# Kernel tuning notes

Hardware: AMD Instinct MI355X
Metric: run time of the kernel (lower is better)

The kernel has to match this reference:

```python
import jax, jax.numpy as jnp
import numpy as np

EMBED = 1024
HEADS = 16
HEAD_DIM = EMBED // HEADS


def setup_inputs() -> dict:
    key = jax.random.key(0)
    k1, k2, k3, k4, k5, k6 = jax.random.split(key, 6)
    N, S = 4, 2048
    return {
        "values": jax.random.normal(k1, (N, S, EMBED), dtype=jnp.float32),
        "keys": jax.random.normal(k2, (N, S, EMBED), dtype=jnp.float32),
        "query": jax.random.normal(k3, (N, S, EMBED), dtype=jnp.float32),
        "mask": jax.random.randint(k4, (N, 1, S, S), 0, 2, dtype=jnp.int32),
        "W_out": jax.random.normal(k5, (EMBED, EMBED), dtype=jnp.float32) * (1.0 / np.sqrt(EMBED)),
        "b_out": jax.random.normal(k6, (EMBED,), dtype=jnp.float32) * 0.01,
    }


def reference(values, keys, query, mask, W_out, b_out):
    N, Q = query.shape[0], query.shape[1]
    K = keys.shape[1]
    v = values.reshape(N, K, HEADS, HEAD_DIM)
    k = keys.reshape(N, K, HEADS, HEAD_DIM)
    q = query.reshape(N, Q, HEADS, HEAD_DIM)
    # [N,H,Q,K] score matrix (materialized, as in the original)
    energy = jnp.einsum("nqhd,nkhd->nhqk", q, k)
    energy = jnp.where(mask == 0, jnp.float32(-1e20), energy)
    # NOTE: original scales by sqrt(embed_size), not sqrt(head_dim)
    attn = jax.nn.softmax(energy / jnp.sqrt(jnp.float32(EMBED)), axis=3)
    out = jnp.einsum("nhqk,nkhd->nqhd", attn, v).reshape(N, Q, EMBED)
    return out @ W_out.T + b_out
```

## Files before the change

### kernel.cpp

```cpp
#include <hip/hip_runtime.h>
#include <stdint.h>

#define SEQ 2048
#define NB 4
#define NHD 16
#define HD 64
#define EMB 1024

typedef unsigned short u16;
typedef unsigned int u32;
typedef unsigned long long u64;
typedef __bf16 bf16x8 __attribute__((ext_vector_type(8)));
typedef float f32x4 __attribute__((ext_vector_type(4)));

__device__ __forceinline__ u16 f2bf(float f) {
    u32 u = __builtin_bit_cast(u32, f);
    u32 r = u + 0x7FFFu + ((u >> 16) & 1u);
    return (u16)(r >> 16);
}

__device__ __forceinline__ float exp2_hw(float x) {
    float r;
    asm("v_exp_f32 %0, %1" : "=v"(r) : "v"(x));
    return r;
}

__device__ __forceinline__ u32 cvtpk_bf16(float lo, float hi) {
    u32 r;
    asm("v_cvt_pk_bf16_f32 %0, %1, %2" : "=v"(r) : "v"(lo), "v"(hi));
    return r;
}

__device__ __forceinline__ void gld16(const void* g, void* l) {
    __builtin_amdgcn_global_load_lds(
        (const __attribute__((address_space(1))) u32*)g,
        (__attribute__((address_space(3))) u32*)l, 16, 0, 0);
}

__global__ void prep_qk(const float* __restrict__ q, const float* __restrict__ k,
                        u16* __restrict__ qb, u16* __restrict__ kb) {
    int tid = blockIdx.x * 256 + threadIdx.x;
    int unit = tid >> 4;
    int dq = (tid & 15) << 2;
    int h = unit & (NHD - 1);
    int ns = unit >> 4;
    int n = ns >> 11, s = ns & (SEQ - 1);
    size_t src = (size_t)ns * EMB + h * HD + dq;
    float4 qv = *(const float4*)(q + src);
    float4 kv = *(const float4*)(k + src);
    size_t dst = ((size_t)(n * NHD + h) * SEQ + s) * HD + dq;
    const float QS = 0.04508422f;
    ushort4 qo, ko;
    qo.x = f2bf(qv.x * QS); qo.y = f2bf(qv.y * QS);
    qo.z = f2bf(qv.z * QS); qo.w = f2bf(qv.w * QS);
    ko.x = f2bf(kv.x); ko.y = f2bf(kv.y); ko.z = f2bf(kv.z); ko.w = f2bf(kv.w);
    *(ushort4*)(qb + dst) = qo;
    *(ushort4*)(kb + dst) = ko;
}

__global__ void prep_v(const float* __restrict__ v, u16* __restrict__ vt) {
    __shared__ float t[64][65];
    int s0 = blockIdx.x << 6, h = blockIdx.y, n = blockIdx.z;
    int tid = threadIdx.x;
    int c = (tid & 15) << 2;
    int r0 = tid >> 4;
#pragma unroll
    for (int it = 0; it < 4; it++) {
        int r = r0 + (it << 4);
        float4 val = *(const float4*)(v + ((size_t)n * SEQ + s0 + r) * EMB + h * HD + c);
        t[c][r] = val.x; t[c + 1][r] = val.y; t[c + 2][r] = val.z; t[c + 3][r] = val.w;
    }
    __syncthreads();
    int d = tid >> 2, so = (tid & 3) << 4;
    size_t dst = ((size_t)(n * NHD + h) * HD + d) * SEQ + s0 + so;
#pragma unroll
    for (int j = 0; j < 4; j++) {
        ushort4 o;
        o.x = f2bf(t[d][so + 4 * j + 0]); o.y = f2bf(t[d][so + 4 * j + 1]);
        o.z = f2bf(t[d][so + 4 * j + 2]); o.w = f2bf(t[d][so + 4 * j + 3]);
        *(ushort4*)(vt + dst + 4 * j) = o;
    }
}

__global__ void prep_mask(const int* __restrict__ m, u64* __restrict__ mb) {
    int gw = (blockIdx.x * 256 + threadIdx.x) >> 6;
    int lane = threadIdx.x & 63;
    int src = ((lane & 12) << 2) | ((lane & 48) >> 2) | (lane & 3);
    for (int i = 0; i < 64; i++) {
        size_t widx = (size_t)gw * 64 + i;
        int v = m[widx * 64 + src];
        u64 b = __ballot(v != 0);
        if (lane == 0) mb[widx] = b;
    }
}

__global__ void prep_w(const float* __restrict__ w, u16* __restrict__ wb) {
    int tid = blockIdx.x * 256 + threadIdx.x;
    float4 v = *(const float4*)(w + (size_t)tid * 4);
    ushort4 o;
    o.x = f2bf(v.x); o.y = f2bf(v.y); o.z = f2bf(v.z); o.w = f2bf(v.w);
    *(ushort4*)(wb + (size_t)tid * 4) = o;
}

__global__ __launch_bounds__(256, 4) void attn_k(
    const u16* __restrict__ qb, const u16* __restrict__ kb,
    const u16* __restrict__ vt, const u64* __restrict__ mbits,
    u16* __restrict__ ao)
{
    __shared__ __align__(16) u16 lds_k[2][64 * 64];
    __shared__ __align__(16) u16 lds_v[2][64 * 64];
    __shared__ __align__(16) u16 lds_p[4][16 * 64];
    const int tid = threadIdx.x;
    const int wave = tid >> 6, lane = tid & 63;
    const int g = lane >> 4, c16 = lane & 15;
    const int bid = blockIdx.x;
    const int swz = (bid & 7) * 256 + (bid >> 3);
    const int n = swz >> 9, h = (swz >> 5) & 15, qt = swz & 31;
    const int qw = (qt << 6) + (wave << 4);
    const size_t nh = (size_t)(n * NHD + h);
    const u16* Qp = qb + nh * SEQ * HD;
    const u16* Kp = kb + nh * SEQ * HD;
    const u16* Vp = vt + nh * HD * SEQ;
    const u64* mrow = mbits + ((size_t)n * SEQ + qw + c16) * (SEQ / 64);

    bf16x8 qa0 = *(const bf16x8*)(Qp + (size_t)(qw + c16) * HD + 8 * g);
    bf16x8 qa1 = *(const bf16x8*)(Qp + (size_t)(qw + c16) * HD + 8 * g + 32);

    f32x4 o[4];
#pragma unroll
    for (int i = 0; i < 4; i++) o[i] = (f32x4){0.f, 0.f, 0.f, 0.f};
    float m_r = -INFINITY, l_r = 0.f;

    auto STAGE = [&](int buf, int kt) {
        int k0 = kt << 6;
#pragma unroll
        for (int i = 0; i < 2; i++) {
            int off = (i << 8) + tid;
            int row = off >> 3;
            int sch = (off & 7) ^ (row & 7);
            int ldso = ((i << 8) + (wave << 6)) << 3;
            gld16(Kp + (size_t)(k0 + row) * HD + (sch << 3), &lds_k[buf][ldso]);
            gld16(Vp + (size_t)row * SEQ + k0 + (sch << 3), &lds_v[buf][ldso]);
        }
    };

    auto COMPUTE = [&](int buf, int kt) {
        u64 mw_cur = mrow[kt];
        u32 mloc = (u32)(mw_cur >> (g << 4)) & 0xFFFFu;
        f32x4 s[4];
#pragma unroll
        for (int t = 0; t < 4; t++)
#pragma unroll
            for (int r = 0; r < 4; r++)
                s[t][r] = ((mloc >> ((t << 2) | r)) & 1u) ? 0.f : -1e20f;
#pragma unroll
        for (int t = 0; t < 4; t++) {
            int kc = (t << 4) + c16;
            int sw = (kc & 7) << 3;
            bf16x8 kf0 = *(const bf16x8*)&lds_k[buf][kc * 64 + ((8 * g) ^ sw)];
            bf16x8 kf1 = *(const bf16x8*)&lds_k[buf][kc * 64 + ((8 * g + 32) ^ sw)];
            s[t] = __builtin_amdgcn_mfma_f32_16x16x32_bf16(kf0, qa0, s[t], 0, 0, 0);
            s[t] = __builtin_amdgcn_mfma_f32_16x16x32_bf16(kf1, qa1, s[t], 0, 0, 0);
        }
        float pmax = fmaxf(fmaxf(fmaxf(s[0][0], s[0][1]), fmaxf(s[0][2], s[0][3])),
                           fmaxf(fmaxf(s[1][0], s[1][1]), fmaxf(s[1][2], s[1][3])));
        pmax = fmaxf(pmax, fmaxf(fmaxf(fmaxf(s[2][0], s[2][1]), fmaxf(s[2][2], s[2][3])),
                                 fmaxf(fmaxf(s[3][0], s[3][1]), fmaxf(s[3][2], s[3][3]))));
        pmax = fmaxf(pmax, __shfl_xor(pmax, 16));
        pmax = fmaxf(pmax, __shfl_xor(pmax, 32));
        if (__ballot(pmax > m_r + 8.f)) {
            float mnew = fmaxf(m_r, pmax);
            float sc = exp2_hw(m_r - mnew);
            m_r = mnew;
            l_r *= sc;
#pragma unroll
            for (int dt = 0; dt < 4; dt++) o[dt] *= sc;
        }
        float ladd = 0.f;
        u32 pk[4][2];
#pragma unroll
        for (int t = 0; t < 4; t++) {
            float p0 = exp2_hw(s[t][0] - m_r);
            float p1 = exp2_hw(s[t][1] - m_r);
            float p2 = exp2_hw(s[t][2] - m_r);
            float p3 = exp2_hw(s[t][3] - m_r);
            ladd += (p0 + p1) + (p2 + p3);
            pk[t][0] = cvtpk_bf16(p0, p1);
            pk[t][1] = cvtpk_bf16(p2, p3);
        }
        ladd += __shfl_xor(ladd, 16);
        ladd += __shfl_xor(ladd, 32);
        l_r += ladd;
        char* pbase = (char*)&lds_p[wave][0];
        int swp = (c16 & 7) << 4;
#pragma unroll
        for (int t = 0; t < 4; t++) {
            u64 w2 = ((u64)pk[t][1] << 32) | pk[t][0];
            *(u64*)(pbase + ((c16 * 128 + 32 * t + 8 * g) ^ swp)) = w2;
        }
        bf16x8 pa0 = *(const bf16x8*)(pbase + ((c16 * 128 + 16 * g) ^ swp));
        bf16x8 pa1 = *(const bf16x8*)(pbase + ((c16 * 128 + 64 + 16 * g) ^ swp));
#pragma unroll
        for (int dt = 0; dt < 4; dt++) {
            int dr = (dt << 4) + c16;
            int swv = (dr & 7) << 3;
            bf16x8 vf0 = *(const bf16x8*)&lds_v[buf][dr * 64 + ((8 * g) ^ swv)];
            bf16x8 vf1 = *(const bf16x8*)&lds_v[buf][dr * 64 + ((8 * g + 32) ^ swv)];
            o[dt] = __builtin_amdgcn_mfma_f32_16x16x32_bf16(vf0, pa0, o[dt], 0, 0, 0);
            o[dt] = __builtin_amdgcn_mfma_f32_16x16x32_bf16(vf1, pa1, o[dt], 0, 0, 0);
        }
    };

    STAGE(0, 0);
    __syncthreads();
    for (int kt = 0; kt < SEQ / 64; kt++) {
        int buf = kt & 1;
        if (kt + 1 < SEQ / 64) STAGE(buf ^ 1, kt + 1);
        COMPUTE(buf, kt);
        __syncthreads();
    }

    float inv = 1.f / l_r;
    size_t obase = ((size_t)n * SEQ + qw + c16) * EMB + h * HD;
#pragma unroll
    for (int dt = 0; dt < 4; dt++) {
        u32 w0 = cvtpk_bf16(o[dt][0] * inv, o[dt][1] * inv);
        u32 w1 = cvtpk_bf16(o[dt][2] * inv, o[dt][3] * inv);
        u64 w2 = ((u64)w1 << 32) | w0;
        *(u64*)(ao + obase + (dt << 4) + (g << 2)) = w2;
    }
}

__global__ __launch_bounds__(256, 2) void proj_k(
    const u16* __restrict__ a, const u16* __restrict__ w,
    const float* __restrict__ bias, float* __restrict__ out)
{
    __shared__ __align__(16) u16 lds_a[2][128 * 64];
    __shared__ __align__(16) u16 lds_b[2][128 * 64];
    const int tid = threadIdx.x;
    const int wave = tid >> 6, lane = tid & 63;
    const int g = lane >> 4, c16 = lane & 15;
    const int m0 = blockIdx.y << 7, n0 = blockIdx.x << 7;
    const int wm = wave >> 1, wn = wave & 1;
    f32x4 acc[4][4];
#pragma unroll
    for (int i = 0; i < 4; i++)
#pragma unroll
        for (int j = 0; j < 4; j++) acc[i][j] = (f32x4){0.f, 0.f, 0.f, 0.f};

    auto STAGE = [&](int buf, int k0) {
#pragma unroll
        for (int i = 0; i < 4; i++) {
            int off = (i << 8) + tid;
            int row = off >> 3;
            int sch = (off & 7) ^ (row & 7);
            int ldso = ((i << 8) + (wave << 6)) << 3;
            gld16(a + (size_t)(m0 + row) * EMB + k0 + (sch << 3), &lds_a[buf][ldso]);
            gld16(w + (size_t)(n0 + row) * EMB + k0 + (sch << 3), &lds_b[buf][ldso]);
        }
    };

    auto COMP = [&](int buf) {
#pragma unroll
        for (int c = 0; c < 2; c++) {
            bf16x8 af[4], bfr[4];
#pragma unroll
            for (int mt = 0; mt < 4; mt++) {
                int row = (wm << 6) + (mt << 4) + c16;
                af[mt] = *(const bf16x8*)&lds_a[buf][row * 64 + ((8 * g + 32 * c) ^ ((row & 7) << 3))];
            }
#pragma unroll
            for (int nt = 0; nt < 4; nt++) {
                int row = (wn << 6) + (nt << 4) + c16;
                bfr[nt] = *(const bf16x8*)&lds_b[buf][row * 64 + ((8 * g + 32 * c) ^ ((row & 7) << 3))];
            }
#pragma unroll
            for (int mt = 0; mt < 4; mt++)
#pragma unroll
                for (int nt = 0; nt < 4; nt++)
                    acc[mt][nt] = __builtin_amdgcn_mfma_f32_16x16x32_bf16(af[mt], bfr[nt], acc[mt][nt], 0, 0, 0);
        }
    };

    STAGE(0, 0);
    __syncthreads();
    for (int ki = 0; ki < EMB / 64; ki++) {
        int buf = ki & 1;
        if (ki + 1 < EMB / 64) STAGE(buf ^ 1, (ki + 1) << 6);
        COMP(buf);
        __syncthreads();
    }

#pragma unroll
    for (int nt = 0; nt < 4; nt++) {
        int col = n0 + (wn << 6) + (nt << 4) + c16;
        float bv = bias[col];
#pragma unroll
        for (int mt = 0; mt < 4; mt++) {
#pragma unroll
            for (int r = 0; r < 4; r++) {
                int row = m0 + (wm << 6) + (mt << 4) + 4 * g + r;
                out[(size_t)row * EMB + col] = acc[mt][nt][r] + bv;
            }
        }
    }
}

extern "C" void kernel_launch(void* const* d_in, const int* in_sizes, int n_in,
                              void* d_out, int out_size, void* d_ws, size_t ws_size,
                              hipStream_t stream) {
    const float* V = (const float*)d_in[0];
    const float* K = (const float*)d_in[1];
    const float* Q = (const float*)d_in[2];
    const int* M = (const int*)d_in[3];
    const float* W = (const float*)d_in[4];
    const float* B = (const float*)d_in[5];
    float* out = (float*)d_out;

    char* ws = (char*)d_ws;
    u16* qb = (u16*)(ws);
    u16* kb = (u16*)(ws + ((size_t)16 << 20));
    u16* vt = (u16*)(ws + ((size_t)32 << 20));
    u64* mb = (u64*)(ws + ((size_t)48 << 20));
    u16* wb = (u16*)(ws + ((size_t)50 << 20));
    u16* ao = (u16*)(ws + ((size_t)52 << 20));

    prep_qk<<<8192, 256, 0, stream>>>(Q, K, qb, kb);
    prep_v<<<dim3(SEQ / 64, NHD, NB), 256, 0, stream>>>(V, vt);
    prep_mask<<<1024, 256, 0, stream>>>(M, mb);
    prep_w<<<1024, 256, 0, stream>>>(W, wb);
    attn_k<<<2048, 256, 0, stream>>>(qb, kb, vt, mb, ao);
    proj_k<<<dim3(EMB / 128, (NB * SEQ) / 128), 256, 0, stream>>>(ao, wb, B, out);
}
```

Baseline: 376.7 us.

## Switch attention to 32x32x16 MFMA with register-resident P via permlane swap

Rewrites the attention kernel to use 32x32x16 bf16 MFMA tiles, with each wave owning 32 queries and each block 128. The score-to-probability handoff now stays in registers through v_permlane32_swap instead of a round trip through a per-wave LDS buffer. The mask bit packing order is changed to match the new accumulator layout. This halves the grid, doubles reuse of each staged K/V tile, and removes LDS traffic for P, at the cost of more accumulator registers and possibly lower occupancy.

Measured after the change: 349.4 us. 7.2% less time.

```diff
diff --git a/kernel.cpp b/kernel.cpp
--- a/kernel.cpp
+++ b/kernel.cpp
@@ -12,6 +12,8 @@
 typedef unsigned long long u64;
 typedef __bf16 bf16x8 __attribute__((ext_vector_type(8)));
 typedef float f32x4 __attribute__((ext_vector_type(4)));
+typedef float f32x16 __attribute__((ext_vector_type(16)));
+typedef u32 u32x4 __attribute__((ext_vector_type(4)));
 
 __device__ __forceinline__ u16 f2bf(float f) {
     u32 u = __builtin_bit_cast(u32, f);
@@ -29,6 +31,10 @@
     u32 r;
     asm("v_cvt_pk_bf16_f32 %0, %1, %2" : "=v"(r) : "v"(lo), "v"(hi));
     return r;
+}
+
+__device__ __forceinline__ void permswap(u32& a, u32& b) {
+    asm volatile("v_permlane32_swap_b32 %0, %1" : "+v"(a), "+v"(b));
 }
 
 __device__ __forceinline__ void gld16(const void* g, void* l) {
@@ -85,7 +91,7 @@
 __global__ void prep_mask(const int* __restrict__ m, u64* __restrict__ mb) {
     int gw = (blockIdx.x * 256 + threadIdx.x) >> 6;
     int lane = threadIdx.x & 63;
-    int src = ((lane & 12) << 2) | ((lane & 48) >> 2) | (lane & 3);
+    int src = (lane & 32) | ((lane & 12) << 1) | ((lane & 16) >> 2) | (lane & 3);
     for (int i = 0; i < 64; i++) {
         size_t widx = (size_t)gw * 64 + i;
         int v = m[widx * 64 + src];
@@ -109,26 +115,27 @@
 {
     __shared__ __align__(16) u16 lds_k[2][64 * 64];
     __shared__ __align__(16) u16 lds_v[2][64 * 64];
-    __shared__ __align__(16) u16 lds_p[4][16 * 64];
     const int tid = threadIdx.x;
     const int wave = tid >> 6, lane = tid & 63;
-    const int g = lane >> 4, c16 = lane & 15;
+    const int l31 = lane & 31, hi = lane >> 5;
     const int bid = blockIdx.x;
-    const int swz = (bid & 7) * 256 + (bid >> 3);
-    const int n = swz >> 9, h = (swz >> 5) & 15, qt = swz & 31;
-    const int qw = (qt << 6) + (wave << 4);
+    const int swz = (bid & 7) * 128 + (bid >> 3);
+    const int n = swz >> 8, h = (swz >> 4) & 15, qt = swz & 15;
+    const int qw = (qt << 7) + (wave << 5);
     const size_t nh = (size_t)(n * NHD + h);
     const u16* Qp = qb + nh * SEQ * HD;
     const u16* Kp = kb + nh * SEQ * HD;
     const u16* Vp = vt + nh * HD * SEQ;
-    const u64* mrow = mbits + ((size_t)n * SEQ + qw + c16) * (SEQ / 64);
-
-    bf16x8 qa0 = *(const bf16x8*)(Qp + (size_t)(qw + c16) * HD + 8 * g);
-    bf16x8 qa1 = *(const bf16x8*)(Qp + (size_t)(qw + c16) * HD + 8 * g + 32);
-
-    f32x4 o[4];
-#pragma unroll
-    for (int i = 0; i < 4; i++) o[i] = (f32x4){0.f, 0.f, 0.f, 0.f};
+    const u64* mrow = mbits + ((size_t)n * SEQ + qw + l31) * (SEQ / 64);
+
+    bf16x8 qa[4];
+#pragma unroll
+    for (int ds = 0; ds < 4; ds++)
+        qa[ds] = *(const bf16x8*)(Qp + (size_t)(qw + l31) * HD + ds * 16 + 8 * hi);
+
+    f32x16 o0 = {0.f}, o1 = {0.f};
+#pragma unroll
+    for (int r = 0; r < 16; r++) { o0[r] = 0.f; o1[r] = 0.f; }
     float m_r = -INFINITY, l_r = 0.f;
 
     auto STAGE = [&](int buf, int kt) {
@@ -145,28 +152,29 @@
     };
 
     auto COMPUTE = [&](int buf, int kt) {
-        u64 mw_cur = mrow[kt];
-        u32 mloc = (u32)(mw_cur >> (g << 4)) & 0xFFFFu;
-        f32x4 s[4];
-#pragma unroll
-        for (int t = 0; t < 4; t++)
-#pragma unroll
-            for (int r = 0; r < 4; r++)
-                s[t][r] = ((mloc >> ((t << 2) | r)) & 1u) ? 0.f : -1e20f;
-#pragma unroll
-        for (int t = 0; t < 4; t++) {
-            int kc = (t << 4) + c16;
-            int sw = (kc & 7) << 3;
-            bf16x8 kf0 = *(const bf16x8*)&lds_k[buf][kc * 64 + ((8 * g) ^ sw)];
-            bf16x8 kf1 = *(const bf16x8*)&lds_k[buf][kc * 64 + ((8 * g + 32) ^ sw)];
-            s[t] = __builtin_amdgcn_mfma_f32_16x16x32_bf16(kf0, qa0, s[t], 0, 0, 0);
-            s[t] = __builtin_amdgcn_mfma_f32_16x16x32_bf16(kf1, qa1, s[t], 0, 0, 0);
-        }
-        float pmax = fmaxf(fmaxf(fmaxf(s[0][0], s[0][1]), fmaxf(s[0][2], s[0][3])),
-                           fmaxf(fmaxf(s[1][0], s[1][1]), fmaxf(s[1][2], s[1][3])));
-        pmax = fmaxf(pmax, fmaxf(fmaxf(fmaxf(s[2][0], s[2][1]), fmaxf(s[2][2], s[2][3])),
-                                 fmaxf(fmaxf(s[3][0], s[3][1]), fmaxf(s[3][2], s[3][3]))));
-        pmax = fmaxf(pmax, __shfl_xor(pmax, 16));
+        u64 mw = mrow[kt];
+        u32 ml0 = (u32)(mw >> (hi << 4)) & 0xFFFFu;
+        u32 ml1 = (u32)(mw >> (32 + (hi << 4))) & 0xFFFFu;
+        f32x16 s0, s1;
+#pragma unroll
+        for (int r = 0; r < 16; r++) {
+            s0[r] = ((ml0 >> r) & 1u) ? 0.f : -1e20f;
+            s1[r] = ((ml1 >> r) & 1u) ? 0.f : -1e20f;
+        }
+        const char* kbase = (const char*)&lds_k[buf][0];
+#pragma unroll
+        for (int ds = 0; ds < 4; ds++) {
+            int c = ((ds << 1) + hi) ^ (l31 & 7);
+            bf16x8 ka0 = *(const bf16x8*)(kbase + l31 * 128 + (c << 4));
+            bf16x8 ka1 = *(const bf16x8*)(kbase + (l31 + 32) * 128 + (c << 4));
+            s0 = __builtin_amdgcn_mfma_f32_32x32x16_bf16(ka0, qa[ds], s0, 0, 0, 0);
+            s1 = __builtin_amdgcn_mfma_f32_32x32x16_bf16(ka1, qa[ds], s1, 0, 0, 0);
+        }
+        float pmax = fmaxf(s0[0], s0[1]);
+#pragma unroll
+        for (int r = 2; r < 16; r++) pmax = fmaxf(pmax, s0[r]);
+#pragma unroll
+        for (int r = 0; r < 16; r++) pmax = fmaxf(pmax, s1[r]);
         pmax = fmaxf(pmax, __shfl_xor(pmax, 32));
         if (__ballot(pmax > m_r + 8.f)) {
             float mnew = fmaxf(m_r, pmax);
@@ -174,40 +182,33 @@
             m_r = mnew;
             l_r *= sc;
 #pragma unroll
-            for (int dt = 0; dt < 4; dt++) o[dt] *= sc;
+            for (int r = 0; r < 16; r++) { o0[r] *= sc; o1[r] *= sc; }
         }
         float ladd = 0.f;
-        u32 pk[4][2];
-#pragma unroll
-        for (int t = 0; t < 4; t++) {
-            float p0 = exp2_hw(s[t][0] - m_r);
-            float p1 = exp2_hw(s[t][1] - m_r);
-            float p2 = exp2_hw(s[t][2] - m_r);
-            float p3 = exp2_hw(s[t][3] - m_r);
-            ladd += (p0 + p1) + (p2 + p3);
-            pk[t][0] = cvtpk_bf16(p0, p1);
-            pk[t][1] = cvtpk_bf16(p2, p3);
-        }
-        ladd += __shfl_xor(ladd, 16);
-        ladd += __shfl_xor(ladd, 32);
+#pragma unroll
+        for (int r = 0; r < 16; r++) { s0[r] = exp2_hw(s0[r] - m_r); ladd += s0[r]; }
+#pragma unroll
+        for (int r = 0; r < 16; r++) { s1[r] = exp2_hw(s1[r] - m_r); ladd += s1[r]; }
         l_r += ladd;
-        char* pbase = (char*)&lds_p[wave][0];
-        int swp = (c16 & 7) << 4;
-#pragma unroll
-        for (int t = 0; t < 4; t++) {
-            u64 w2 = ((u64)pk[t][1] << 32) | pk[t][0];
-            *(u64*)(pbase + ((c16 * 128 + 32 * t + 8 * g) ^ swp)) = w2;
-        }
-        bf16x8 pa0 = *(const bf16x8*)(pbase + ((c16 * 128 + 16 * g) ^ swp));
-        bf16x8 pa1 = *(const bf16x8*)(pbase + ((c16 * 128 + 64 + 16 * g) ^ swp));
-#pragma unroll
-        for (int dt = 0; dt < 4; dt++) {
-            int dr = (dt << 4) + c16;
-            int swv = (dr & 7) << 3;
-            bf16x8 vf0 = *(const bf16x8*)&lds_v[buf][dr * 64 + ((8 * g) ^ swv)];
-            bf16x8 vf1 = *(const bf16x8*)&lds_v[buf][dr * 64 + ((8 * g + 32) ^ swv)];
-            o[dt] = __builtin_amdgcn_mfma_f32_16x16x32_bf16(vf0, pa0, o[dt], 0, 0, 0);
-            o[dt] = __builtin_amdgcn_mfma_f32_16x16x32_bf16(vf1, pa1, o[dt], 0, 0, 0);
+        u32 w[16];
+#pragma unroll
+        for (int i = 0; i < 8; i++) w[i] = cvtpk_bf16(s0[2 * i], s0[2 * i + 1]);
+#pragma unroll
+        for (int i = 0; i < 8; i++) w[8 + i] = cvtpk_bf16(s1[2 * i], s1[2 * i + 1]);
+        permswap(w[0], w[2]);  permswap(w[1], w[3]);
+        permswap(w[4], w[6]);  permswap(w[5], w[7]);
+        permswap(w[8], w[10]); permswap(w[9], w[11]);
+        permswap(w[12], w[14]); permswap(w[13], w[15]);
+        const char* vbase = (const char*)&lds_v[buf][0];
+#pragma unroll
+        for (int ks = 0; ks < 4; ks++) {
+            u32x4 t = {w[4 * ks], w[4 * ks + 1], w[4 * ks + 2], w[4 * ks + 3]};
+            bf16x8 pb = __builtin_bit_cast(bf16x8, t);
+            int c = ((ks << 1) + hi) ^ (l31 & 7);
+            bf16x8 va0 = *(const bf16x8*)(vbase + l31 * 128 + (c << 4));
+            bf16x8 va1 = *(const bf16x8*)(vbase + (l31 + 32) * 128 + (c << 4));
+            o0 = __builtin_amdgcn_mfma_f32_32x32x16_bf16(va0, pb, o0, 0, 0, 0);
+            o1 = __builtin_amdgcn_mfma_f32_32x32x16_bf16(va1, pb, o1, 0, 0, 0);
         }
     };
 
@@ -220,14 +221,17 @@
         __syncthreads();
     }
 
+    l_r += __shfl_xor(l_r, 32);
     float inv = 1.f / l_r;
-    size_t obase = ((size_t)n * SEQ + qw + c16) * EMB + h * HD;
-#pragma unroll
-    for (int dt = 0; dt < 4; dt++) {
-        u32 w0 = cvtpk_bf16(o[dt][0] * inv, o[dt][1] * inv);
-        u32 w1 = cvtpk_bf16(o[dt][2] * inv, o[dt][3] * inv);
-        u64 w2 = ((u64)w1 << 32) | w0;
-        *(u64*)(ao + obase + (dt << 4) + (g << 2)) = w2;
+    size_t ob = ((size_t)n * SEQ + qw + l31) * EMB + h * HD;
+#pragma unroll
+    for (int rq = 0; rq < 4; rq++) {
+        u32 a0 = cvtpk_bf16(o0[4 * rq] * inv, o0[4 * rq + 1] * inv);
+        u32 b0 = cvtpk_bf16(o0[4 * rq + 2] * inv, o0[4 * rq + 3] * inv);
+        *(u64*)(ao + ob + 8 * rq + 4 * hi) = ((u64)b0 << 32) | a0;
+        u32 a1 = cvtpk_bf16(o1[4 * rq] * inv, o1[4 * rq + 1] * inv);
+        u32 b1 = cvtpk_bf16(o1[4 * rq + 2] * inv, o1[4 * rq + 3] * inv);
+        *(u64*)(ao + ob + 32 + 8 * rq + 4 * hi) = ((u64)b1 << 32) | a1;
     }
 }
 
@@ -329,6 +333,6 @@
     prep_v<<<dim3(SEQ / 64, NHD, NB), 256, 0, stream>>>(V, vt);
     prep_mask<<<1024, 256, 0, stream>>>(M, mb);
     prep_w<<<1024, 256, 0, stream>>>(W, wb);
-    attn_k<<<2048, 256, 0, stream>>>(qb, kb, vt, mb, ao);
+    attn_k<<<1024, 256, 0, stream>>>(qb, kb, vt, mb, ao);
     proj_k<<<dim3(EMB / 128, (NB * SEQ) / 128), 256, 0, stream>>>(ao, wb, B, out);
 }
```
